# Optimization experiments

Hardware: AMD Instinct MI355X
Metric: run time of the kernel (lower is better)

## Reference

```python
import jax, jax.numpy as jnp
import numpy as np

HEADS = 16
DIM_HEAD = 64
SCALE = 8.0
NUM_NULL_KV = 2
NON_CAUSAL_PREFIX = 64
LN_EPS = 1e-5

def _l2norm(t):
    # F.normalize: t / max(||t||_2, eps)
    n = jnp.sqrt(jnp.sum(t * t, axis=-1, keepdims=True))
    return t / jnp.maximum(n, 1e-12)

def _layer_norm(x, gamma):
    mu = jnp.mean(x, axis=-1, keepdims=True)
    var = jnp.mean((x - mu) ** 2, axis=-1, keepdims=True)
    return (x - mu) * jax.lax.rsqrt(var + LN_EPS) * gamma  # beta buffer is zeros

def setup_inputs() -> dict:
    key = jax.random.key(0)
    ks = jax.random.split(key, 6)
    b, n, dim = 2, 2048, 1024
    inner = HEADS * DIM_HEAD
    return {
        "x": jax.random.normal(ks[0], (b, n, dim), jnp.float32),
        "gamma": jnp.ones((dim,), jnp.float32),
        "Wq": jax.random.normal(ks[1], (dim, inner), jnp.float32) * (dim ** -0.5),
        "Wkv": jax.random.normal(ks[2], (dim, 2 * DIM_HEAD), jnp.float32) * (dim ** -0.5),
        "q_scale": jnp.ones((DIM_HEAD,), jnp.float32),
        "k_scale": jnp.ones((DIM_HEAD,), jnp.float32),
        "null_kv": jax.random.normal(ks[3], (2, NUM_NULL_KV, DIM_HEAD), jnp.float32),
        "Wout": jax.random.normal(ks[4], (inner, dim), jnp.float32) * (inner ** -0.5),
    }

def reference(x, gamma, Wq, Wkv, q_scale, k_scale, null_kv, Wout):
    b, n, dim = x.shape
    # NOTE: in the torch module, kv_input = x BEFORE self.norm is applied
    kv = jnp.einsum('bnd,de->bne', x, Wkv)          # [b, n, 2*dh]
    k, v = kv[..., :DIM_HEAD], kv[..., DIM_HEAD:]    # single shared kv head (MQA)
    xn = _layer_norm(x, gamma)
    q = jnp.einsum('bnd,de->bne', xn, Wq)            # [b, n, h*dh]
    # null kv prepended
    null_k = jnp.broadcast_to(null_kv[0], (b, NUM_NULL_KV, DIM_HEAD))
    null_v = jnp.broadcast_to(null_kv[1], (b, NUM_NULL_KV, DIM_HEAD))
    k = jnp.concatenate([null_k, k], axis=1)         # [b, j, dh]
    v = jnp.concatenate([null_v, v], axis=1)
    q = q.reshape(b, n, HEADS, DIM_HEAD).transpose(0, 2, 1, 3)  # [b, h, n, dh]
    q = _l2norm(q) * q_scale
    k = _l2norm(k) * k_scale
    sim = jnp.einsum('bhid,bjd->bhij', q, k) * SCALE  # [b, h, i, j]
    i, j = n, k.shape[1]
    rows = jnp.arange(i)[:, None]
    cols = jnp.arange(j)[None, :]
    causal_mask = cols > rows + (j - i)               # triu(j - i + 1)
    prefix_free = (rows < NON_CAUSAL_PREFIX) & (cols < NON_CAUSAL_PREFIX + (j - i))
    causal_mask = causal_mask & (~prefix_free)
    neg = -jnp.finfo(sim.dtype).max
    sim = jnp.where(causal_mask, neg, sim)
    attn = jax.nn.softmax(sim, axis=-1)
    out = jnp.einsum('bhij,bjd->bhid', attn, v)       # [b, h, n, dh]
    out = out.transpose(0, 2, 1, 3).reshape(b, n, HEADS * DIM_HEAD)
    return jnp.einsum('bne,ed->bnd', out, Wout)
```

## Files before the change

kernel.cpp:

```cpp
#include <hip/hip_runtime.h>

typedef _Float16 h16;
typedef _Float16 f16x8 __attribute__((ext_vector_type(8)));
typedef _Float16 f16x4 __attribute__((ext_vector_type(4)));
typedef float f32x4 __attribute__((ext_vector_type(4)));

#define KSCALE_FOLD 11.541560327111707f

__global__ __launch_bounds__(256) void prep_w(const float* __restrict__ Wq,
    const float* __restrict__ Wkv, const float* __restrict__ Wout,
    const float* __restrict__ gamma, h16* __restrict__ W1t, h16* __restrict__ Wot,
    float* __restrict__ cq)
{
    __shared__ float ts[64][65];
    int bx = blockIdx.x, by = blockIdx.y;
    int c = threadIdx.x & 63, rc = threadIdx.x >> 6;
    const float* src; int ld, scol, drow0; h16* dst; bool useg = false;
    if (by < 16)      { src = Wq;   ld = 1024; scol = by*64;       dst = W1t; drow0 = scol;        useg = true; }
    else if (by < 18) { src = Wkv;  ld = 128;  scol = (by-16)*64;  dst = W1t; drow0 = 1024 + scol; }
    else              { src = Wout; ld = 1024; scol = (by-18)*64;  dst = Wot; drow0 = scol; }
    float part = 0.f;
#pragma unroll
    for (int i = 0; i < 16; ++i) {
        int r = rc*16 + i;
        float v = src[(size_t)(bx*64 + r)*ld + scol + c];
        if (useg) v *= gamma[bx*64 + r];
        part += v;
        ts[r][c] = v;
    }
    if (useg) atomicAdd(&cq[scol + c], part);
    __syncthreads();
#pragma unroll
    for (int i = 0; i < 16; ++i) {
        int r = rc*16 + i;
        dst[(size_t)(drow0 + r)*1024 + bx*64 + c] = (h16)ts[c][r];
    }
}

__global__ __launch_bounds__(256) void stats_k(const float* __restrict__ x,
    float* __restrict__ mu, float* __restrict__ rr, h16* __restrict__ xh)
{
    int w = threadIdx.x >> 6, l = threadIdx.x & 63;
    int row = blockIdx.x*4 + w;
    const float* xr = x + (size_t)row*1024;
    float s = 0.f, ss = 0.f;
    float4 v[4];
#pragma unroll
    for (int i = 0; i < 4; ++i) {
        v[i] = *(const float4*)(xr + i*256 + l*4);
        s  += v[i].x + v[i].y + v[i].z + v[i].w;
        ss += v[i].x*v[i].x + v[i].y*v[i].y + v[i].z*v[i].z + v[i].w*v[i].w;
    }
#pragma unroll
    for (int m = 1; m < 64; m <<= 1) { s += __shfl_xor(s, m); ss += __shfl_xor(ss, m); }
    float m_ = s * (1.f/1024.f);
    float var = ss * (1.f/1024.f) - m_*m_;
    float r_ = rsqrtf(var + 1e-5f);
    if (l == 0) { mu[row] = m_; rr[row] = r_; }
    h16* xo = xh + (size_t)row*1024;
#pragma unroll
    for (int i = 0; i < 4; ++i) {
        f16x4 hv = { (h16)v[i].x, (h16)v[i].y, (h16)v[i].z, (h16)v[i].w };
        *(f16x4*)(xo + i*256 + l*4) = hv;
    }
}

__global__ __launch_bounds__(256) void null_k(const float* __restrict__ nkv,
    const float* __restrict__ kscale, h16* __restrict__ Kh, h16* __restrict__ Vth)
{
    int tid = threadIdx.x;
    if (blockIdx.x == 0 && tid < 128) {
        int t = tid >> 6, d = tid & 63;
        float kv = nkv[(0*2 + t)*64 + d];
        float ss = kv*kv;
#pragma unroll
        for (int m = 1; m < 64; m <<= 1) ss += __shfl_xor(ss, m);
        float inv = 1.f / fmaxf(sqrtf(ss), 1e-12f);
        h16 kvh = (h16)(kv * inv * kscale[d] * KSCALE_FOLD);
        Kh[(size_t)(0*2112 + t)*64 + d] = kvh;
        Kh[(size_t)(1*2112 + t)*64 + d] = kvh;
        float nv = nkv[(2 + t)*64 + d];
        Vth[(size_t)(0*64 + d)*2112 + t] = (h16)nv;
        Vth[(size_t)(1*64 + d)*2112 + t] = (h16)nv;
    }
    for (int idx = blockIdx.x*256 + tid; idx < 2*62*64; idx += 2048) {
        int b = idx / (62*64), rem = idx % (62*64);
        int j = 2050 + rem/64, d = rem & 63;
        Kh[((size_t)b*2112 + j)*64 + d] = (h16)0.f;
        Vth[((size_t)b*64 + d)*2112 + j] = (h16)0.f;
    }
}

template<int MODE>
__global__ __launch_bounds__(256) void gemm_k(
    const h16* __restrict__ A, const h16* __restrict__ B,
    const float* __restrict__ mu, const float* __restrict__ rr, const float* __restrict__ cq,
    const float* __restrict__ qscale, const float* __restrict__ kscale,
    h16* __restrict__ Qh, h16* __restrict__ Kh, h16* __restrict__ Vth, float* __restrict__ outp)
{
    __shared__ h16 As[2][128*64];
    __shared__ h16 Bs[2][64*64];
    int tid = threadIdx.x;
    int w = tid >> 6, l = tid & 63;
    int lq = l & 15, qq = l >> 4;
    int arow0 = blockIdx.y*128, bcol0 = blockIdx.x*64;
    const int K = 1024;
    f32x4 acc[2][4] = {};

    auto STAGE = [&](int buf, int kt) {
#pragma unroll
        for (int i = 0; i < 4; ++i) {
            int s = i*256 + tid;
            int row = s >> 3;
            int cb = ((s & 7)*16) ^ ((row & 7) << 4);
            const char* asrc = (const char*)(A + (size_t)(arow0 + row)*K + kt) + cb;
            __builtin_amdgcn_global_load_lds(
                (const __attribute__((address_space(1))) unsigned int*)asrc,
                (__attribute__((address_space(3))) unsigned int*)((char*)&As[buf][0] + s*16), 16, 0, 0);
        }
#pragma unroll
        for (int i = 0; i < 2; ++i) {
            int s = i*256 + tid;
            int row = s >> 3;
            int cb = ((s & 7)*16) ^ ((row & 7) << 4);
            const char* bsrc = (const char*)(B + (size_t)(bcol0 + row)*K + kt) + cb;
            __builtin_amdgcn_global_load_lds(
                (const __attribute__((address_space(1))) unsigned int*)bsrc,
                (__attribute__((address_space(3))) unsigned int*)((char*)&Bs[buf][0] + s*16), 16, 0, 0);
        }
    };

    STAGE(0, 0);
    int cur = 0;
    for (int kt = 0; kt < K; kt += 64) {
        int nkt = (kt + 64 < K) ? kt + 64 : kt;
        STAGE(cur ^ 1, nkt);
        asm volatile("s_waitcnt vmcnt(6)" ::: "memory");
        __builtin_amdgcn_s_barrier();
        __builtin_amdgcn_sched_barrier(0);
        const char* Ab = (const char*)&As[cur][0];
        const char* Bb = (const char*)&Bs[cur][0];
#pragma unroll
        for (int kc = 0; kc < 2; ++kc) {
            int cb = (kc*64 + qq*16) ^ ((lq & 7) << 4);
            f16x8 af[2], bf[4];
#pragma unroll
            for (int mt = 0; mt < 2; ++mt)
                af[mt] = *(const f16x8*)(Ab + (w*32 + mt*16 + lq)*128 + cb);
#pragma unroll
            for (int nt = 0; nt < 4; ++nt)
                bf[nt] = *(const f16x8*)(Bb + (nt*16 + lq)*128 + cb);
#pragma unroll
            for (int mt = 0; mt < 2; ++mt)
#pragma unroll
                for (int nt = 0; nt < 4; ++nt)
                    acc[mt][nt] = __builtin_amdgcn_mfma_f32_16x16x32_f16(af[mt], bf[nt], acc[mt][nt], 0, 0, 0);
        }
        __builtin_amdgcn_sched_barrier(0);
        __builtin_amdgcn_s_barrier();
        cur ^= 1;
    }
    asm volatile("s_waitcnt vmcnt(0)" ::: "memory");

    int wrow0 = arow0 + w*32;
    int bx = blockIdx.x;
    if (MODE == 1) {
#pragma unroll
        for (int mt = 0; mt < 2; ++mt)
#pragma unroll
            for (int nt = 0; nt < 4; ++nt)
#pragma unroll
                for (int i = 0; i < 4; ++i)
                    outp[(size_t)(wrow0 + mt*16 + qq*4 + i)*1024 + bcol0 + nt*16 + lq] = acc[mt][nt][i];
        return;
    }
    if (bx < 16) {
        float cqv[4], qs[4];
#pragma unroll
        for (int nt = 0; nt < 4; ++nt) {
            cqv[nt] = cq[bcol0 + nt*16 + lq];
            qs[nt] = qscale[nt*16 + lq];
        }
#pragma unroll
        for (int mt = 0; mt < 2; ++mt) {
            float muv[4], rv[4], ssq[4], qv[4][4];
#pragma unroll
            for (int i = 0; i < 4; ++i) {
                int row = wrow0 + mt*16 + qq*4 + i;
                muv[i] = mu[row]; rv[i] = rr[row]; ssq[i] = 0.f;
            }
#pragma unroll
            for (int nt = 0; nt < 4; ++nt)
#pragma unroll
                for (int i = 0; i < 4; ++i) {
                    float q = rv[i]*(acc[mt][nt][i] - muv[i]*cqv[nt]);
                    qv[nt][i] = q; ssq[i] += q*q;
                }
#pragma unroll
            for (int i = 0; i < 4; ++i) {
                float s2 = ssq[i];
                s2 += __shfl_xor(s2, 1); s2 += __shfl_xor(s2, 2);
                s2 += __shfl_xor(s2, 4); s2 += __shfl_xor(s2, 8);
                ssq[i] = 1.f / fmaxf(sqrtf(s2), 1e-12f);
            }
#pragma unroll
            for (int nt = 0; nt < 4; ++nt)
#pragma unroll
                for (int i = 0; i < 4; ++i) {
                    int row = wrow0 + mt*16 + qq*4 + i;
                    Qh[(size_t)row*1024 + bcol0 + nt*16 + lq] = (h16)(qv[nt][i]*ssq[i]*qs[nt]);
                }
        }
    } else if (bx == 16) {
        float ks[4];
#pragma unroll
        for (int nt = 0; nt < 4; ++nt) ks[nt] = kscale[nt*16 + lq] * KSCALE_FOLD;
#pragma unroll
        for (int mt = 0; mt < 2; ++mt) {
            float ssq[4] = {0.f, 0.f, 0.f, 0.f};
#pragma unroll
            for (int nt = 0; nt < 4; ++nt)
#pragma unroll
                for (int i = 0; i < 4; ++i) ssq[i] += acc[mt][nt][i]*acc[mt][nt][i];
#pragma unroll
            for (int i = 0; i < 4; ++i) {
                float s2 = ssq[i];
                s2 += __shfl_xor(s2, 1); s2 += __shfl_xor(s2, 2);
                s2 += __shfl_xor(s2, 4); s2 += __shfl_xor(s2, 8);
                ssq[i] = 1.f / fmaxf(sqrtf(s2), 1e-12f);
            }
#pragma unroll
            for (int nt = 0; nt < 4; ++nt)
#pragma unroll
                for (int i = 0; i < 4; ++i) {
                    int row = wrow0 + mt*16 + qq*4 + i;
                    int b = row >> 11, ii = row & 2047;
                    Kh[((size_t)b*2112 + 2 + ii)*64 + nt*16 + lq] = (h16)(acc[mt][nt][i]*ssq[i]*ks[nt]);
                }
        }
    } else {
#pragma unroll
        for (int mt = 0; mt < 2; ++mt)
#pragma unroll
            for (int nt = 0; nt < 4; ++nt)
#pragma unroll
                for (int i = 0; i < 4; ++i) {
                    int row = wrow0 + mt*16 + qq*4 + i;
                    int b = row >> 11, ii = row & 2047;
                    Vth[((size_t)b*64 + nt*16 + lq)*2112 + 2 + ii] = (h16)acc[mt][nt][i];
                }
    }
}

__global__ __launch_bounds__(512) void attn_k(const h16* __restrict__ Qh,
    const h16* __restrict__ Kh, const h16* __restrict__ Vth, h16* __restrict__ Oh)
{
    __shared__ h16 KVs[2][2][64*64];
    __shared__ h16 Ps[8][16*64];
    int id = blockIdx.x;
    int u = id >> 5;
    int qt = (u < 16) ? u : 47 - u;
    int bh = id & 31;
    int b = bh >> 4, h = bh & 15;
    int tid = threadIdx.x, w = tid >> 6, l = tid & 63;
    int g = w >> 2, wq = w & 3;
    int lq = l & 15, qq = l >> 4;
    int qstart = qt * 64;
    int q0w = qstart + wq * 16;
    h16* P = &Ps[w][0];
    int xs = (lq & 7) << 4;

    f16x8 qf[2];
#pragma unroll
    for (int kc = 0; kc < 2; ++kc)
        qf[kc] = *(const f16x8*)(Qh + (size_t)(b*2048 + q0w + lq)*1024 + h*64 + kc*32 + qq*8);

    int qrow = q0w + lq;
    int thr = (qrow < 64) ? 65 : qrow + 2;

    int cbs = ((tid & 7)*16) ^ (((tid >> 3) & 7) << 4);
    const char* ksrc = (const char*)(Kh + (size_t)b*2112*64) + (size_t)(tid >> 3)*128 + cbs;
    const char* vsrc = (const char*)(Vth + (size_t)b*64*2112) + (size_t)(tid >> 3)*4224 + cbs;

    f32x4 oacc[4] = {};
    float lrun = 0.f;

    int lastc = qstart + 65;
    if (lastc > 2049) lastc = 2049;
    int ntile = lastc/64 + 1;

    auto STAGE = [&](int buf, int kv0) {
        __builtin_amdgcn_global_load_lds(
            (const __attribute__((address_space(1))) unsigned int*)(ksrc + (size_t)kv0*128),
            (__attribute__((address_space(3))) unsigned int*)(&KVs[buf][0][w*512]), 16, 0, 0);
        __builtin_amdgcn_global_load_lds(
            (const __attribute__((address_space(1))) unsigned int*)(vsrc + (size_t)kv0*2),
            (__attribute__((address_space(3))) unsigned int*)(&KVs[buf][1][w*512]), 16, 0, 0);
    };

    STAGE(0, 0);
    int cur = 0;
    for (int t = 0; t < ntile; ++t) {
        int kv0 = t*64;
        int nxt = (t + 1 < ntile) ? t + 1 : t;
        STAGE(cur ^ 1, nxt*64);
        asm volatile("s_waitcnt vmcnt(2)" ::: "memory");
        __builtin_amdgcn_s_barrier();
        __builtin_amdgcn_sched_barrier(0);

        int kv0g = kv0 + g*32;
        bool active = (kv0g <= q0w + 17) || (q0w < 64 && kv0g < 66);
        if (active) {
            const char* Kl = (const char*)&KVs[cur][0][0];
            const char* Vl = (const char*)&KVs[cur][1][0];
            f32x4 s[2] = {};
#pragma unroll
            for (int kc = 0; kc < 2; ++kc) {
                int ko = (kc*64 + qq*16) ^ xs;
                f16x8 kf0 = *(const f16x8*)(Kl + ((g*2+0)*16 + lq)*128 + ko);
                f16x8 kf1 = *(const f16x8*)(Kl + ((g*2+1)*16 + lq)*128 + ko);
                s[0] = __builtin_amdgcn_mfma_f32_16x16x32_f16(kf0, qf[kc], s[0], 0, 0, 0);
                s[1] = __builtin_amdgcn_mfma_f32_16x16x32_f16(kf1, qf[kc], s[1], 0, 0, 0);
            }
            if (kv0g + 31 > q0w + 2) {
#pragma unroll
                for (int mt = 0; mt < 2; ++mt)
#pragma unroll
                    for (int i = 0; i < 4; ++i) {
                        int kv = kv0g + mt*16 + qq*4 + i;
                        if (kv > thr) s[mt][i] = -__builtin_inff();
                    }
            }
            float ps = 0.f;
#pragma unroll
            for (int mt = 0; mt < 2; ++mt)
#pragma unroll
                for (int i = 0; i < 4; ++i) {
                    float p = exp2f(s[mt][i]);
                    s[mt][i] = p; ps += p;
                }
            ps += __shfl_xor(ps, 16);
            ps += __shfl_xor(ps, 32);
            lrun += ps;
#pragma unroll
            for (int mt = 0; mt < 2; ++mt) {
                uint2 pk;
                pk.x = __builtin_bit_cast(unsigned int, __builtin_amdgcn_cvt_pkrtz(s[mt][0], s[mt][1]));
                pk.y = __builtin_bit_cast(unsigned int, __builtin_amdgcn_cvt_pkrtz(s[mt][2], s[mt][3]));
                *(uint2*)((char*)P + lq*128 + ((mt*32 + qq*8) ^ xs)) = pk;
            }
            f16x8 pf = *(const f16x8*)((const char*)P + lq*128 + ((qq*16) ^ xs));
            int kov = (g*64 + qq*16) ^ xs;
#pragma unroll
            for (int dm = 0; dm < 4; ++dm) {
                f16x8 vf = *(const f16x8*)(Vl + (dm*16 + lq)*128 + kov);
                oacc[dm] = __builtin_amdgcn_mfma_f32_16x16x32_f16(vf, pf, oacc[dm], 0, 0, 0);
            }
        }
        __builtin_amdgcn_sched_barrier(0);
        __builtin_amdgcn_s_barrier();
        cur ^= 1;
    }
    asm volatile("s_waitcnt vmcnt(0)" ::: "memory");
    __syncthreads();

    float* Om = (float*)&KVs[0][0][0];
    float* Lm = (float*)&Ps[0][0];
    if (g == 1) {
#pragma unroll
        for (int dm = 0; dm < 4; ++dm)
            *(f32x4*)(Om + wq*1024 + lq*64 + dm*16 + qq*4) = oacc[dm];
        if (qq == 0) Lm[wq*16 + lq] = lrun;
    }
    __syncthreads();
    if (g == 0) {
        float ltot = lrun + Lm[wq*16 + lq];
        float inv = 1.f / ltot;
#pragma unroll
        for (int dm = 0; dm < 4; ++dm) {
            f32x4 po = *(const f32x4*)(Om + wq*1024 + lq*64 + dm*16 + qq*4);
            f16x4 ov;
#pragma unroll
            for (int i = 0; i < 4; ++i) ov[i] = (h16)((oacc[dm][i] + po[i]) * inv);
            *(f16x4*)(Oh + (size_t)(b*2048 + q0w + lq)*1024 + h*64 + dm*16 + qq*4) = ov;
        }
    }
}

extern "C" void kernel_launch(void* const* d_in, const int* in_sizes, int n_in,
                              void* d_out, int out_size, void* d_ws, size_t ws_size,
                              hipStream_t stream)
{
    const float* x      = (const float*)d_in[0];
    const float* gamma  = (const float*)d_in[1];
    const float* Wq     = (const float*)d_in[2];
    const float* Wkv    = (const float*)d_in[3];
    const float* qscale = (const float*)d_in[4];
    const float* kscale = (const float*)d_in[5];
    const float* nkv    = (const float*)d_in[6];
    const float* Wout   = (const float*)d_in[7];
    float* out = (float*)d_out;
    char* ws = (char*)d_ws;

    h16* xh   = (h16*)(ws);
    h16* Qh   = (h16*)(ws + 8388608);
    h16* Oh   = (h16*)(ws + 16777216);
    h16* W1t  = (h16*)(ws + 25165824);
    h16* Wot  = (h16*)(ws + 27525120);
    h16* Kh   = (h16*)(ws + 29622272);
    h16* Vth  = (h16*)(ws + 30162944);
    float* cq = (float*)(ws + 30703616);
    float* mu = (float*)(ws + 30707712);
    float* rr = (float*)(ws + 30724096);

    hipMemsetAsync(cq, 0, 4096, stream);
    prep_w<<<dim3(16, 34), 256, 0, stream>>>(Wq, Wkv, Wout, gamma, W1t, Wot, cq);
    stats_k<<<dim3(1024), 256, 0, stream>>>(x, mu, rr, xh);
    null_k<<<dim3(8), 256, 0, stream>>>(nkv, kscale, Kh, Vth);
    gemm_k<0><<<dim3(18, 32), 256, 0, stream>>>(xh, W1t, mu, rr, cq, qscale, kscale, Qh, Kh, Vth, out);
    attn_k<<<dim3(1024), 512, 0, stream>>>(Qh, Kh, Vth, Oh);
    gemm_k<1><<<dim3(16, 32), 256, 0, stream>>>(Oh, Wot, mu, rr, cq, qscale, kscale, Qh, Kh, Vth, out);
}
```

Measured before the change: 100.7 us.

## Share K/V tiles across two heads per attention block and merge prep kernels

The attention kernel now has each 512-thread block cover two heads for the same query tile. The two groups of four waves share one staged K/V tile, exploiting the single shared MQA kv head, instead of splitting the 64-key tile between the groups and reducing partial outputs through LDS at the end. This halves the block count and global K/V traffic and removes the cross-group reduction and extra syncs, at the cost of more per-wave MFMA work and registers. The three preprocessing kernels are also fused into one launch to cut launch overhead.

```diff
diff --git a/kernel.cpp b/kernel.cpp
--- a/kernel.cpp
+++ b/kernel.cpp
@@ -7,87 +7,86 @@
 
 #define KSCALE_FOLD 11.541560327111707f
 
-__global__ __launch_bounds__(256) void prep_w(const float* __restrict__ Wq,
+__global__ __launch_bounds__(256) void pre_k(const float* __restrict__ Wq,
     const float* __restrict__ Wkv, const float* __restrict__ Wout,
-    const float* __restrict__ gamma, h16* __restrict__ W1t, h16* __restrict__ Wot,
-    float* __restrict__ cq)
+    const float* __restrict__ gamma, const float* __restrict__ x,
+    const float* __restrict__ nkv, const float* __restrict__ kscale,
+    h16* __restrict__ W1t, h16* __restrict__ Wot, float* __restrict__ cq,
+    float* __restrict__ mu, float* __restrict__ rr, h16* __restrict__ xh,
+    h16* __restrict__ Kh, h16* __restrict__ Vth)
 {
     __shared__ float ts[64][65];
-    int bx = blockIdx.x, by = blockIdx.y;
-    int c = threadIdx.x & 63, rc = threadIdx.x >> 6;
-    const float* src; int ld, scol, drow0; h16* dst; bool useg = false;
-    if (by < 16)      { src = Wq;   ld = 1024; scol = by*64;       dst = W1t; drow0 = scol;        useg = true; }
-    else if (by < 18) { src = Wkv;  ld = 128;  scol = (by-16)*64;  dst = W1t; drow0 = 1024 + scol; }
-    else              { src = Wout; ld = 1024; scol = (by-18)*64;  dst = Wot; drow0 = scol; }
-    float part = 0.f;
-#pragma unroll
-    for (int i = 0; i < 16; ++i) {
-        int r = rc*16 + i;
-        float v = src[(size_t)(bx*64 + r)*ld + scol + c];
-        if (useg) v *= gamma[bx*64 + r];
-        part += v;
-        ts[r][c] = v;
-    }
-    if (useg) atomicAdd(&cq[scol + c], part);
-    __syncthreads();
-#pragma unroll
-    for (int i = 0; i < 16; ++i) {
-        int r = rc*16 + i;
-        dst[(size_t)(drow0 + r)*1024 + bx*64 + c] = (h16)ts[c][r];
-    }
-}
-
-__global__ __launch_bounds__(256) void stats_k(const float* __restrict__ x,
-    float* __restrict__ mu, float* __restrict__ rr, h16* __restrict__ xh)
-{
-    int w = threadIdx.x >> 6, l = threadIdx.x & 63;
-    int row = blockIdx.x*4 + w;
-    const float* xr = x + (size_t)row*1024;
-    float s = 0.f, ss = 0.f;
-    float4 v[4];
-#pragma unroll
-    for (int i = 0; i < 4; ++i) {
-        v[i] = *(const float4*)(xr + i*256 + l*4);
-        s  += v[i].x + v[i].y + v[i].z + v[i].w;
-        ss += v[i].x*v[i].x + v[i].y*v[i].y + v[i].z*v[i].z + v[i].w*v[i].w;
-    }
-#pragma unroll
-    for (int m = 1; m < 64; m <<= 1) { s += __shfl_xor(s, m); ss += __shfl_xor(ss, m); }
-    float m_ = s * (1.f/1024.f);
-    float var = ss * (1.f/1024.f) - m_*m_;
-    float r_ = rsqrtf(var + 1e-5f);
-    if (l == 0) { mu[row] = m_; rr[row] = r_; }
-    h16* xo = xh + (size_t)row*1024;
-#pragma unroll
-    for (int i = 0; i < 4; ++i) {
-        f16x4 hv = { (h16)v[i].x, (h16)v[i].y, (h16)v[i].z, (h16)v[i].w };
-        *(f16x4*)(xo + i*256 + l*4) = hv;
-    }
-}
-
-__global__ __launch_bounds__(256) void null_k(const float* __restrict__ nkv,
-    const float* __restrict__ kscale, h16* __restrict__ Kh, h16* __restrict__ Vth)
-{
+    int pid = blockIdx.x;
     int tid = threadIdx.x;
-    if (blockIdx.x == 0 && tid < 128) {
-        int t = tid >> 6, d = tid & 63;
-        float kv = nkv[(0*2 + t)*64 + d];
-        float ss = kv*kv;
-#pragma unroll
-        for (int m = 1; m < 64; m <<= 1) ss += __shfl_xor(ss, m);
-        float inv = 1.f / fmaxf(sqrtf(ss), 1e-12f);
-        h16 kvh = (h16)(kv * inv * kscale[d] * KSCALE_FOLD);
-        Kh[(size_t)(0*2112 + t)*64 + d] = kvh;
-        Kh[(size_t)(1*2112 + t)*64 + d] = kvh;
-        float nv = nkv[(2 + t)*64 + d];
-        Vth[(size_t)(0*64 + d)*2112 + t] = (h16)nv;
-        Vth[(size_t)(1*64 + d)*2112 + t] = (h16)nv;
-    }
-    for (int idx = blockIdx.x*256 + tid; idx < 2*62*64; idx += 2048) {
-        int b = idx / (62*64), rem = idx % (62*64);
-        int j = 2050 + rem/64, d = rem & 63;
-        Kh[((size_t)b*2112 + j)*64 + d] = (h16)0.f;
-        Vth[((size_t)b*64 + d)*2112 + j] = (h16)0.f;
+    if (pid < 544) {
+        int bx = pid & 15, by = pid >> 4;
+        int c = tid & 63, rc = tid >> 6;
+        const float* src; int ld, scol, drow0; h16* dst; bool useg = false;
+        if (by < 16)      { src = Wq;   ld = 1024; scol = by*64;       dst = W1t; drow0 = scol;        useg = true; }
+        else if (by < 18) { src = Wkv;  ld = 128;  scol = (by-16)*64;  dst = W1t; drow0 = 1024 + scol; }
+        else              { src = Wout; ld = 1024; scol = (by-18)*64;  dst = Wot; drow0 = scol; }
+        float part = 0.f;
+#pragma unroll
+        for (int i = 0; i < 16; ++i) {
+            int r = rc*16 + i;
+            float v = src[(size_t)(bx*64 + r)*ld + scol + c];
+            if (useg) v *= gamma[bx*64 + r];
+            part += v;
+            ts[r][c] = v;
+        }
+        if (useg) atomicAdd(&cq[scol + c], part);
+        __syncthreads();
+#pragma unroll
+        for (int i = 0; i < 16; ++i) {
+            int r = rc*16 + i;
+            dst[(size_t)(drow0 + r)*1024 + bx*64 + c] = (h16)ts[c][r];
+        }
+    } else if (pid < 1568) {
+        int w = tid >> 6, l = tid & 63;
+        int row = (pid - 544)*4 + w;
+        const float* xr = x + (size_t)row*1024;
+        float s = 0.f, ss = 0.f;
+        float4 v[4];
+#pragma unroll
+        for (int i = 0; i < 4; ++i) {
+            v[i] = *(const float4*)(xr + i*256 + l*4);
+            s  += v[i].x + v[i].y + v[i].z + v[i].w;
+            ss += v[i].x*v[i].x + v[i].y*v[i].y + v[i].z*v[i].z + v[i].w*v[i].w;
+        }
+#pragma unroll
+        for (int m = 1; m < 64; m <<= 1) { s += __shfl_xor(s, m); ss += __shfl_xor(ss, m); }
+        float m_ = s * (1.f/1024.f);
+        float var = ss * (1.f/1024.f) - m_*m_;
+        float r_ = rsqrtf(var + 1e-5f);
+        if (l == 0) { mu[row] = m_; rr[row] = r_; }
+        h16* xo = xh + (size_t)row*1024;
+#pragma unroll
+        for (int i = 0; i < 4; ++i) {
+            f16x4 hv = { (h16)v[i].x, (h16)v[i].y, (h16)v[i].z, (h16)v[i].w };
+            *(f16x4*)(xo + i*256 + l*4) = hv;
+        }
+    } else {
+        int nb = pid - 1568;
+        if (nb == 0 && tid < 128) {
+            int t = tid >> 6, d = tid & 63;
+            float kv = nkv[(0*2 + t)*64 + d];
+            float ss = kv*kv;
+#pragma unroll
+            for (int m = 1; m < 64; m <<= 1) ss += __shfl_xor(ss, m);
+            float inv = 1.f / fmaxf(sqrtf(ss), 1e-12f);
+            h16 kvh = (h16)(kv * inv * kscale[d] * KSCALE_FOLD);
+            Kh[(size_t)(0*2112 + t)*64 + d] = kvh;
+            Kh[(size_t)(1*2112 + t)*64 + d] = kvh;
+            float nv = nkv[(2 + t)*64 + d];
+            Vth[(size_t)(0*64 + d)*2112 + t] = (h16)nv;
+            Vth[(size_t)(1*64 + d)*2112 + t] = (h16)nv;
+        }
+        for (int idx = nb*256 + tid; idx < 2*62*64; idx += 2048) {
+            int b = idx / (62*64), rem = idx % (62*64);
+            int j = 2050 + rem/64, d = rem & 63;
+            Kh[((size_t)b*2112 + j)*64 + d] = (h16)0.f;
+            Vth[((size_t)b*64 + d)*2112 + j] = (h16)0.f;
+        }
     }
 }
 
@@ -252,18 +251,19 @@
     }
 }
 
-__global__ __launch_bounds__(512) void attn_k(const h16* __restrict__ Qh,
+__global__ __launch_bounds__(512, 4) void attn_k(const h16* __restrict__ Qh,
     const h16* __restrict__ Kh, const h16* __restrict__ Vth, h16* __restrict__ Oh)
 {
     __shared__ h16 KVs[2][2][64*64];
     __shared__ h16 Ps[8][16*64];
     int id = blockIdx.x;
-    int u = id >> 5;
+    int hp = id & 7;
+    int b = (id >> 3) & 1;
+    int u = id >> 4;
     int qt = (u < 16) ? u : 47 - u;
-    int bh = id & 31;
-    int b = bh >> 4, h = bh & 15;
     int tid = threadIdx.x, w = tid >> 6, l = tid & 63;
-    int g = w >> 2, wq = w & 3;
+    int h = hp*2 + (w >> 2);
+    int wq = w & 3;
     int lq = l & 15, qq = l >> 4;
     int qstart = qt * 64;
     int q0w = qstart + wq * 16;
@@ -278,24 +278,24 @@
     int qrow = q0w + lq;
     int thr = (qrow < 64) ? 65 : qrow + 2;
 
-    int cbs = ((tid & 7)*16) ^ (((tid >> 3) & 7) << 4);
-    const char* ksrc = (const char*)(Kh + (size_t)b*2112*64) + (size_t)(tid >> 3)*128 + cbs;
-    const char* vsrc = (const char*)(Vth + (size_t)b*64*2112) + (size_t)(tid >> 3)*4224 + cbs;
+    int srow = tid >> 3;
+    int cbs = ((tid & 7)*16) ^ ((srow & 7) << 4);
+    const char* ksrc = (const char*)(Kh + (size_t)b*2112*64) + (size_t)srow*128 + cbs;
+    const char* vsrc = (const char*)(Vth + (size_t)b*64*2112) + (size_t)srow*4224 + cbs;
 
     f32x4 oacc[4] = {};
     float lrun = 0.f;
 
     int lastc = qstart + 65;
-    if (lastc > 2049) lastc = 2049;
     int ntile = lastc/64 + 1;
 
     auto STAGE = [&](int buf, int kv0) {
         __builtin_amdgcn_global_load_lds(
             (const __attribute__((address_space(1))) unsigned int*)(ksrc + (size_t)kv0*128),
-            (__attribute__((address_space(3))) unsigned int*)(&KVs[buf][0][w*512]), 16, 0, 0);
+            (__attribute__((address_space(3))) unsigned int*)((char*)&KVs[buf][0][0] + tid*16), 16, 0, 0);
         __builtin_amdgcn_global_load_lds(
             (const __attribute__((address_space(1))) unsigned int*)(vsrc + (size_t)kv0*2),
-            (__attribute__((address_space(3))) unsigned int*)(&KVs[buf][1][w*512]), 16, 0, 0);
+            (__attribute__((address_space(3))) unsigned int*)((char*)&KVs[buf][1][0] + tid*16), 16, 0, 0);
     };
 
     STAGE(0, 0);
@@ -308,32 +308,34 @@
         __builtin_amdgcn_s_barrier();
         __builtin_amdgcn_sched_barrier(0);
 
-        int kv0g = kv0 + g*32;
-        bool active = (kv0g <= q0w + 17) || (q0w < 64 && kv0g < 66);
+        bool active = (kv0 <= q0w + 17) || (q0w < 64 && kv0 < 66);
         if (active) {
             const char* Kl = (const char*)&KVs[cur][0][0];
             const char* Vl = (const char*)&KVs[cur][1][0];
-            f32x4 s[2] = {};
+            f32x4 s[4] = {};
 #pragma unroll
             for (int kc = 0; kc < 2; ++kc) {
                 int ko = (kc*64 + qq*16) ^ xs;
-                f16x8 kf0 = *(const f16x8*)(Kl + ((g*2+0)*16 + lq)*128 + ko);
-                f16x8 kf1 = *(const f16x8*)(Kl + ((g*2+1)*16 + lq)*128 + ko);
-                s[0] = __builtin_amdgcn_mfma_f32_16x16x32_f16(kf0, qf[kc], s[0], 0, 0, 0);
-                s[1] = __builtin_amdgcn_mfma_f32_16x16x32_f16(kf1, qf[kc], s[1], 0, 0, 0);
-            }
-            if (kv0g + 31 > q0w + 2) {
-#pragma unroll
-                for (int mt = 0; mt < 2; ++mt)
+                f16x8 kf[4];
+#pragma unroll
+                for (int mt = 0; mt < 4; ++mt)
+                    kf[mt] = *(const f16x8*)(Kl + (mt*16 + lq)*128 + ko);
+#pragma unroll
+                for (int mt = 0; mt < 4; ++mt)
+                    s[mt] = __builtin_amdgcn_mfma_f32_16x16x32_f16(kf[mt], qf[kc], s[mt], 0, 0, 0);
+            }
+            if (kv0 + 63 > q0w + 2) {
+#pragma unroll
+                for (int mt = 0; mt < 4; ++mt)
 #pragma unroll
                     for (int i = 0; i < 4; ++i) {
-                        int kv = kv0g + mt*16 + qq*4 + i;
+                        int kv = kv0 + mt*16 + qq*4 + i;
                         if (kv > thr) s[mt][i] = -__builtin_inff();
                     }
             }
             float ps = 0.f;
 #pragma unroll
-            for (int mt = 0; mt < 2; ++mt)
+            for (int mt = 0; mt < 4; ++mt)
 #pragma unroll
                 for (int i = 0; i < 4; ++i) {
                     float p = exp2f(s[mt][i]);
@@ -343,18 +345,21 @@
             ps += __shfl_xor(ps, 32);
             lrun += ps;
 #pragma unroll
-            for (int mt = 0; mt < 2; ++mt) {
+            for (int mt = 0; mt < 4; ++mt) {
                 uint2 pk;
                 pk.x = __builtin_bit_cast(unsigned int, __builtin_amdgcn_cvt_pkrtz(s[mt][0], s[mt][1]));
                 pk.y = __builtin_bit_cast(unsigned int, __builtin_amdgcn_cvt_pkrtz(s[mt][2], s[mt][3]));
                 *(uint2*)((char*)P + lq*128 + ((mt*32 + qq*8) ^ xs)) = pk;
             }
-            f16x8 pf = *(const f16x8*)((const char*)P + lq*128 + ((qq*16) ^ xs));
-            int kov = (g*64 + qq*16) ^ xs;
-#pragma unroll
-            for (int dm = 0; dm < 4; ++dm) {
-                f16x8 vf = *(const f16x8*)(Vl + (dm*16 + lq)*128 + kov);
-                oacc[dm] = __builtin_amdgcn_mfma_f32_16x16x32_f16(vf, pf, oacc[dm], 0, 0, 0);
+#pragma unroll
+            for (int kc = 0; kc < 2; ++kc) {
+                int ko = (kc*64 + qq*16) ^ xs;
+                f16x8 pf = *(const f16x8*)((const char*)P + lq*128 + ko);
+#pragma unroll
+                for (int dm = 0; dm < 4; ++dm) {
+                    f16x8 vf = *(const f16x8*)(Vl + (dm*16 + lq)*128 + ko);
+                    oacc[dm] = __builtin_amdgcn_mfma_f32_16x16x32_f16(vf, pf, oacc[dm], 0, 0, 0);
+                }
             }
         }
         __builtin_amdgcn_sched_barrier(0);
@@ -362,28 +367,14 @@
         cur ^= 1;
     }
     asm volatile("s_waitcnt vmcnt(0)" ::: "memory");
-    __syncthreads();
-
-    float* Om = (float*)&KVs[0][0][0];
-    float* Lm = (float*)&Ps[0][0];
-    if (g == 1) {
-#pragma unroll
-        for (int dm = 0; dm < 4; ++dm)
-            *(f32x4*)(Om + wq*1024 + lq*64 + dm*16 + qq*4) = oacc[dm];
-        if (qq == 0) Lm[wq*16 + lq] = lrun;
-    }
-    __syncthreads();
-    if (g == 0) {
-        float ltot = lrun + Lm[wq*16 + lq];
-        float inv = 1.f / ltot;
-#pragma unroll
-        for (int dm = 0; dm < 4; ++dm) {
-            f32x4 po = *(const f32x4*)(Om + wq*1024 + lq*64 + dm*16 + qq*4);
-            f16x4 ov;
-#pragma unroll
-            for (int i = 0; i < 4; ++i) ov[i] = (h16)((oacc[dm][i] + po[i]) * inv);
-            *(f16x4*)(Oh + (size_t)(b*2048 + q0w + lq)*1024 + h*64 + dm*16 + qq*4) = ov;
-        }
+
+    float inv = 1.f / lrun;
+#pragma unroll
+    for (int dm = 0; dm < 4; ++dm) {
+        f16x4 ov;
+#pragma unroll
+        for (int i = 0; i < 4; ++i) ov[i] = (h16)(oacc[dm][i]*inv);
+        *(f16x4*)(Oh + (size_t)(b*2048 + q0w + lq)*1024 + h*64 + dm*16 + qq*4) = ov;
     }
 }
 
@@ -414,10 +405,9 @@
     float* rr = (float*)(ws + 30724096);
 
     hipMemsetAsync(cq, 0, 4096, stream);
-    prep_w<<<dim3(16, 34), 256, 0, stream>>>(Wq, Wkv, Wout, gamma, W1t, Wot, cq);
-    stats_k<<<dim3(1024), 256, 0, stream>>>(x, mu, rr, xh);
-    null_k<<<dim3(8), 256, 0, stream>>>(nkv, kscale, Kh, Vth);
+    pre_k<<<dim3(1576), 256, 0, stream>>>(Wq, Wkv, Wout, gamma, x, nkv, kscale,
+                                          W1t, Wot, cq, mu, rr, xh, Kh, Vth);
     gemm_k<0><<<dim3(18, 32), 256, 0, stream>>>(xh, W1t, mu, rr, cq, qscale, kscale, Qh, Kh, Vth, out);
-    attn_k<<<dim3(1024), 512, 0, stream>>>(Qh, Kh, Vth, Oh);
+    attn_k<<<dim3(512), 512, 0, stream>>>(Qh, Kh, Vth, Oh);
     gemm_k<1><<<dim3(16, 32), 256, 0, stream>>>(Oh, Wot, mu, rr, cq, qscale, kscale, Qh, Kh, Vth, out);
 }
```

After: 102.3 us. Within noise of the previous version (+1.6%).
